# Kernel tuning notes

Measured on AMD Instinct MI355X. Metric: run time of the kernel, lower is better.

Reference implementation:

```python
import jax, jax.numpy as jnp
import numpy as np

K = 3            # kernel_size
H = 2048
W = 2048
N = 1_000_000    # number of query points
LATENT = 4
POS = 6
CTRL = 2
HID = 64
OUT = 4
IN_CH = (LATENT + POS + CTRL) * K * K  # 108


def _linear_params(key, fan_in, fan_out):
    bound = 1.0 / np.sqrt(fan_in)
    kw, kb = jax.random.split(key)
    Wm = jax.random.uniform(kw, (fan_in, fan_out), minval=-bound, maxval=bound, dtype=jnp.float32)
    bm = jax.random.uniform(kb, (fan_out,), minval=-bound, maxval=bound, dtype=jnp.float32)
    return Wm, bm


def setup_inputs() -> dict:
    key = jax.random.key(0)
    ks = jax.random.split(key, 7)
    W1, b1 = _linear_params(ks[0], IN_CH, HID)
    W2, b2 = _linear_params(ks[1], HID, 2 * HID)
    W3, b3 = _linear_params(ks[2], 2 * HID, HID)
    W4, b4 = _linear_params(ks[3], HID, OUT)
    latent = jax.random.normal(ks[4], (H, W, LATENT), dtype=jnp.float32)
    raw_pos = jax.random.randint(ks[5], (N, 2), 0, W).astype(jnp.int32)  # (x, y) coords
    control = jax.random.normal(ks[6], (N, CTRL), dtype=jnp.float32)
    return {"latent": latent, "raw_pos": raw_pos, "control": control,
            "W1": W1, "b1": b1, "W2": W2, "b2": b2,
            "W3": W3, "b3": b3, "W4": W4, "b4": b4}


def reference(latent, raw_pos, control, W1, b1, W2, b2, W3, b3, W4, b4):
    Hh, Ww, C = latent.shape
    n = raw_pos.shape[0]
    r = K // 2
    d = jnp.arange(-r, r + 1, dtype=raw_pos.dtype)
    ox, oy = jnp.meshgrid(d, d, indexing="xy")
    offsets = jnp.stack([ox.ravel(), oy.ravel()], axis=-1)          # [K*K, 2] (dx, dy)
    exp = raw_pos[:, None, :] + offsets[None, :, :]                 # [N, K*K, 2]
    ex = jnp.clip(exp[..., 0], 0, Ww - 1)
    ey = jnp.clip(exp[..., 1], 0, Hh - 1)
    lin = ey * Ww + ex                                              # linear gather indices
    latent_values = latent.reshape(-1, C)[lin]                      # [N, K*K, C] irregular gather

    xs = jnp.clip(raw_pos[:, 0:1], 0, Ww - 1).astype(latent.dtype) / Ww
    ys = jnp.clip(raw_pos[:, 1:2], 0, Hh - 1).astype(latent.dtype) / Hh
    tp = jnp.asarray(2.0 * np.pi, latent.dtype)
    # sinusoidal encoding with input included: [x, y, sin(2pi x), cos(2pi x), sin(2pi y), cos(2pi y)] -> pos_channels=6
    pos = jnp.concatenate([xs, ys, jnp.sin(tp * xs), jnp.cos(tp * xs), jnp.sin(tp * ys), jnp.cos(tp * ys)], axis=-1)
    pos_e = jnp.broadcast_to(pos[:, None, :], (n, K * K, POS))
    ctl_e = jnp.broadcast_to(control[:, None, :], (n, K * K, control.shape[-1]))

    patches = jnp.concatenate([latent_values, pos_e, ctl_e], axis=-1)  # [N, K*K, 12]
    x = patches.reshape(n, -1)                                          # [N, 108]

    h = jax.nn.gelu(x @ W1 + b1, approximate=False)
    h = jax.nn.gelu(h @ W2 + b2, approximate=False)
    h = jax.nn.gelu(h @ W3 + b3, approximate=False)
    return jax.nn.sigmoid(h @ W4 + b4)                                  # [N, 4]
```

## Files before the change

kernel.cpp:

```cpp
#include <hip/hip_runtime.h>
#include <hip/hip_fp16.h>

typedef __attribute__((ext_vector_type(8))) _Float16 half8;
typedef __attribute__((ext_vector_type(4))) float f32x4;
typedef __attribute__((ext_vector_type(4))) unsigned int uint4v;

#define HGT 2048
#define WID 2048
#define NPTS 1000000
#define NTILES 3907
#define WBYTES 44096
#define BIAS_OFF 43008

__device__ __host__ inline int c64map(int k){
  return 16*(k>>5) + 32*((k&7)>>2) + 4*((k>>3)&3) + (k&3);
}
__device__ __host__ inline int c128map(int k){
  return 16*(k>>5) + 64*((k&7)>>2) + 4*((k>>3)&3) + (k&3);
}

__global__ void prepack_kernel(const float* __restrict__ W1, const float* __restrict__ b1,
                               const float* __restrict__ W2, const float* __restrict__ b2,
                               const float* __restrict__ W3, const float* __restrict__ b3,
                               const float* __restrict__ W4, const float* __restrict__ b4,
                               unsigned short* __restrict__ packed){
  int tid = blockIdx.x*256 + threadIdx.x;
  if (tid < 42*64) {
    int f = tid >> 6, l = tid & 63;
    int fr = l & 15, kg = l >> 4;
    int layer, mt, kk;
    if (f < 8)       { layer=1; mt=f>>1;      kk=f&1; }
    else if (f < 24) { layer=2; mt=(f-8)>>1;  kk=(f-8)&1; }
    else if (f < 40) { layer=3; mt=(f-24)>>2; kk=(f-24)&3; }
    else             { layer=4; mt=0;         kk=f-40; }
    unsigned short v16[8];
    #pragma unroll
    for (int e=0;e<8;e++){
      int k = kk*32 + kg*8 + e;
      int fout = mt*16 + fr;
      float v = 0.0f;
      if (layer==1) {
        if (k < 36)      { v = W1[((k>>2)*12 + (k&3))*64 + fout]; }
        else if (k < 42) { float s=0.f; for (int p=0;p<9;p++) s += W1[(p*12+4+(k-36))*64 + fout]; v=s; }
        else if (k < 44) { float s=0.f; for (int p=0;p<9;p++) s += W1[(p*12+10+(k-42))*64 + fout]; v=s; }
      } else if (layer==2) { v = W2[c64map(k)*128 + fout]; }
      else if (layer==3)   { v = W3[c128map(k)*64 + fout]; }
      else                 { v = (fr < 4) ? W4[c64map(k)*4 + fr] : 0.0f; }
      v16[e] = __half_as_ushort(__float2half(v));
    }
    unsigned short* dst = packed + (size_t)f*512 + (size_t)l*8;
    #pragma unroll
    for (int e=0;e<8;e++) dst[e] = v16[e];
  }
  int bt = tid - 42*64;
  if (bt >= 0 && bt < 272) {
    float v;
    if (bt < 64)       v = b1[bt];
    else if (bt < 192) v = b2[bt-64];
    else if (bt < 256) v = b3[bt-192];
    else               v = (bt-256 < 4) ? b4[bt-256] : 0.0f;
    ((float*)((char*)packed + BIAS_OFF))[bt] = v;
  }
}

__device__ inline unsigned pkf(float a, float b){
  return __builtin_bit_cast(unsigned, __builtin_amdgcn_cvt_pkrtz(a, b));
}
__device__ inline float gelu1(float x){
  const float x2 = x*x;
  const float z  = x * __builtin_fmaf(0.10294913f, x2, 2.3021164f);
  const float t  = __builtin_amdgcn_exp2f(z);
  const float r  = __builtin_amdgcn_rcpf(t + 1.0f);
  return __builtin_fmaf(-x, r, x);
}
__device__ inline unsigned gelu2_v(float a, float b){
  return pkf(gelu1(a), gelu1(b));
}
__device__ inline float fast_sigmoid(float x){
  return __builtin_amdgcn_rcpf(1.0f + __builtin_amdgcn_exp2f(-1.442695041f*x));
}

template<int MT,int KT,int DKT,int FB,int BO>
__device__ inline void layer2(const half8* __restrict__ Wfrag, const float* __restrict__ bias,
                              const uint4v* ia, const uint4v* ib,
                              uint4v* oa, uint4v* ob, int lane, int g){
  #pragma unroll
  for (int mt=0; mt<MT; mt++){
    const f32x4 bv = *(const f32x4*)(bias + BO + mt*16 + g*4);
    f32x4 a = bv, b = bv;
    #pragma unroll
    for (int kk=0; kk<KT; kk++){
      const half8 w = Wfrag[(FB + mt*KT + kk)*64 + lane];
      a = __builtin_amdgcn_mfma_f32_16x16x32_f16(w, __builtin_bit_cast(half8, ia[kk]), a, 0,0,0);
      b = __builtin_amdgcn_mfma_f32_16x16x32_f16(w, __builtin_bit_cast(half8, ib[kk]), b, 0,0,0);
    }
    oa[mt%DKT][(mt/DKT)*2+0] = gelu2_v(a[0], a[1]);
    oa[mt%DKT][(mt/DKT)*2+1] = gelu2_v(a[2], a[3]);
    ob[mt%DKT][(mt/DKT)*2+0] = gelu2_v(b[0], b[1]);
    ob[mt%DKT][(mt/DKT)*2+1] = gelu2_v(b[2], b[3]);
  }
}

__global__ __launch_bounds__(512, 6)
void decoder_kernel(const float* __restrict__ latent, const int* __restrict__ raw_pos,
                    const float* __restrict__ control, const unsigned short* __restrict__ packed,
                    float* __restrict__ out){
  __shared__ __attribute__((aligned(16))) char smem[WBYTES];
  const int tid = threadIdx.x;
  {
    const f32x4* src = (const f32x4*)packed;
    f32x4* dst = (f32x4*)smem;
    for (int i = tid; i < WBYTES/16; i += 512) dst[i] = src[i];
  }
  __syncthreads();

  const half8* Wfrag = (const half8*)smem;
  const float* bias  = (const float*)(smem + BIAS_OFF);
  const int wave = tid >> 6, lane = tid & 63;
  const int nlo = lane & 15, g = lane >> 4;
  const int pA = g*2, pB = g*2+1;
  const int qA = (pA>=3) + (pA>=6), qB = (pB>=3) + (pB>=6);
  const int dyA = qA-1, dxA = pA-3*qA-1;
  const int dyB = qB-1, dxB = pB-3*qB-1;

  const int tile = blockIdx.x;
  const int R0 = tile*256 + wave*32;
  if (R0 >= NPTS) return;

  uint4v bx0[2], bx1[2];
  #pragma unroll
  for (int jj=0; jj<2; jj++){
    const int prow = R0 + jj*16 + nlo;
    const int2 xy = ((const int2*)raw_pos)[prow];
    const int exA = min(max(xy.x + dxA, 0), WID-1);
    const int eyA = min(max(xy.y + dyA, 0), HGT-1);
    const int exB = min(max(xy.x + dxB, 0), WID-1);
    const int eyB = min(max(xy.y + dyB, 0), HGT-1);
    const f32x4 lA = *(const f32x4*)(latent + ((size_t)eyA*WID + exA)*4);
    const f32x4 lB = *(const f32x4*)(latent + ((size_t)eyB*WID + exB)*4);
    uint4v f0;
    f0.x = pkf(lA[0], lA[1]); f0.y = pkf(lA[2], lA[3]);
    f0.z = pkf(lB[0], lB[1]); f0.w = pkf(lB[2], lB[3]);

    const float xs = (float)xy.x * (1.0f/WID), ys = (float)xy.y * (1.0f/HGT);
    const float sx = __builtin_amdgcn_sinf(xs), cx = __builtin_amdgcn_cosf(xs);
    const float sy = __builtin_amdgcn_sinf(ys), cy = __builtin_amdgcn_cosf(ys);
    uint4v f1; f1.x = 0u; f1.y = 0u; f1.z = 0u; f1.w = 0u;
    if (g == 0){
      const int ex8 = min(xy.x + 1, WID-1), ey8 = min(xy.y + 1, HGT-1);
      const f32x4 l8 = *(const f32x4*)(latent + ((size_t)ey8*WID + ex8)*4);
      f1.x = pkf(l8[0], l8[1]); f1.y = pkf(l8[2], l8[3]);
      f1.z = pkf(xs, ys); f1.w = pkf(sx, cx);
    } else if (g == 1){
      const float2 ct = ((const float2*)control)[prow];
      f1.x = pkf(sy, cy); f1.y = pkf(ct.x, ct.y);
    }
    if (jj == 0){ bx0[0] = f0; bx0[1] = f1; }
    else        { bx1[0] = f0; bx1[1] = f1; }
  }

  uint4v h1a[2], h1b[2], h2a[4], h2b[4], h3a[2], h3b[2];
  layer2<4,2,2, 0,  0>(Wfrag, bias, bx0, bx1, h1a, h1b, lane, g);
  layer2<8,2,4, 8, 64>(Wfrag, bias, h1a, h1b, h2a, h2b, lane, g);
  layer2<4,4,2,24,192>(Wfrag, bias, h2a, h2b, h3a, h3b, lane, g);

  const f32x4 bv4 = *(const f32x4*)(bias + 256 + g*4);
  f32x4 a = bv4, b = bv4;
  #pragma unroll
  for (int kk=0; kk<2; kk++){
    const half8 w = Wfrag[(40+kk)*64 + lane];
    a = __builtin_amdgcn_mfma_f32_16x16x32_f16(w, __builtin_bit_cast(half8, h3a[kk]), a, 0,0,0);
    b = __builtin_amdgcn_mfma_f32_16x16x32_f16(w, __builtin_bit_cast(half8, h3b[kk]), b, 0,0,0);
  }
  if (g == 0){
    f32x4 oa, ob;
    #pragma unroll
    for (int j=0;j<4;j++){ oa[j] = fast_sigmoid(a[j]); ob[j] = fast_sigmoid(b[j]); }
    *(f32x4*)(out + (size_t)(R0 + nlo)*4)      = oa;
    *(f32x4*)(out + (size_t)(R0 + 16 + nlo)*4) = ob;
  }
}

extern "C" void kernel_launch(void* const* d_in, const int* in_sizes, int n_in,
                              void* d_out, int out_size, void* d_ws, size_t ws_size,
                              hipStream_t stream) {
  const float* latent  = (const float*)d_in[0];
  const int*   raw_pos = (const int*)d_in[1];
  const float* control = (const float*)d_in[2];
  const float* W1 = (const float*)d_in[3];
  const float* b1 = (const float*)d_in[4];
  const float* W2 = (const float*)d_in[5];
  const float* b2 = (const float*)d_in[6];
  const float* W3 = (const float*)d_in[7];
  const float* b3 = (const float*)d_in[8];
  const float* W4 = (const float*)d_in[9];
  const float* b4 = (const float*)d_in[10];
  unsigned short* packed = (unsigned short*)d_ws;

  prepack_kernel<<<12, 256, 0, stream>>>(W1,b1,W2,b2,W3,b3,W4,b4,packed);
  decoder_kernel<<<NTILES, 512, 0, stream>>>(latent, raw_pos, control, packed, (float*)d_out);
}
```

Baseline: 108.3 us.

## Process 64 points per wave to amortize weight fragment loads

Each wave now handles four 16-point groups instead of two, so every weight fragment read from LDS feeds four MFMAs instead of two. The grid is halved and occupancy bounds drop from 6 to 4 waves per SIMD to fit the larger register footprint. Tail handling clamps input rows and guards output stores. This cuts LDS weight traffic and the per-block weight staging cost, but lowers occupancy, which may hurt latency hiding for the random latent gathers.

```diff
diff --git a/kernel.cpp b/kernel.cpp
--- a/kernel.cpp
+++ b/kernel.cpp
@@ -8,7 +8,7 @@
 #define HGT 2048
 #define WID 2048
 #define NPTS 1000000
-#define NTILES 3907
+#define NTILES 1954
 #define WBYTES 44096
 #define BIAS_OFF 43008
 
@@ -80,28 +80,32 @@
   return __builtin_amdgcn_rcpf(1.0f + __builtin_amdgcn_exp2f(-1.442695041f*x));
 }
 
-template<int MT,int KT,int DKT,int FB,int BO>
-__device__ inline void layer2(const half8* __restrict__ Wfrag, const float* __restrict__ bias,
-                              const uint4v* ia, const uint4v* ib,
-                              uint4v* oa, uint4v* ob, int lane, int g){
+template<int MT,int KT,int DKT,int FB,int BO,int J,int KIN>
+__device__ __forceinline__ void layerJ(const half8* __restrict__ Wfrag, const float* __restrict__ bias,
+                                       const uint4v (&in)[J][KIN], uint4v (&outp)[J][DKT],
+                                       int lane, int g){
   #pragma unroll
   for (int mt=0; mt<MT; mt++){
     const f32x4 bv = *(const f32x4*)(bias + BO + mt*16 + g*4);
-    f32x4 a = bv, b = bv;
+    f32x4 acc[J];
+    #pragma unroll
+    for (int j=0;j<J;j++) acc[j] = bv;
     #pragma unroll
     for (int kk=0; kk<KT; kk++){
       const half8 w = Wfrag[(FB + mt*KT + kk)*64 + lane];
-      a = __builtin_amdgcn_mfma_f32_16x16x32_f16(w, __builtin_bit_cast(half8, ia[kk]), a, 0,0,0);
-      b = __builtin_amdgcn_mfma_f32_16x16x32_f16(w, __builtin_bit_cast(half8, ib[kk]), b, 0,0,0);
-    }
-    oa[mt%DKT][(mt/DKT)*2+0] = gelu2_v(a[0], a[1]);
-    oa[mt%DKT][(mt/DKT)*2+1] = gelu2_v(a[2], a[3]);
-    ob[mt%DKT][(mt/DKT)*2+0] = gelu2_v(b[0], b[1]);
-    ob[mt%DKT][(mt/DKT)*2+1] = gelu2_v(b[2], b[3]);
-  }
-}
-
-__global__ __launch_bounds__(512, 6)
+      #pragma unroll
+      for (int j=0;j<J;j++)
+        acc[j] = __builtin_amdgcn_mfma_f32_16x16x32_f16(w, __builtin_bit_cast(half8, in[j][kk]), acc[j], 0,0,0);
+    }
+    #pragma unroll
+    for (int j=0;j<J;j++){
+      outp[j][mt%DKT][(mt/DKT)*2+0] = gelu2_v(acc[j][0], acc[j][1]);
+      outp[j][mt%DKT][(mt/DKT)*2+1] = gelu2_v(acc[j][2], acc[j][3]);
+    }
+  }
+}
+
+__global__ __launch_bounds__(512, 4)
 void decoder_kernel(const float* __restrict__ latent, const int* __restrict__ raw_pos,
                     const float* __restrict__ control, const unsigned short* __restrict__ packed,
                     float* __restrict__ out){
@@ -123,14 +127,12 @@
   const int dyA = qA-1, dxA = pA-3*qA-1;
   const int dyB = qB-1, dxB = pB-3*qB-1;
 
-  const int tile = blockIdx.x;
-  const int R0 = tile*256 + wave*32;
-  if (R0 >= NPTS) return;
-
-  uint4v bx0[2], bx1[2];
-  #pragma unroll
-  for (int jj=0; jj<2; jj++){
-    const int prow = R0 + jj*16 + nlo;
+  const int R0 = blockIdx.x*512 + wave*64;
+
+  uint4v bx[4][2];
+  #pragma unroll
+  for (int jj=0; jj<4; jj++){
+    const int prow = min(R0 + jj*16 + nlo, NPTS-1);
     const int2 xy = ((const int2*)raw_pos)[prow];
     const int exA = min(max(xy.x + dxA, 0), WID-1);
     const int eyA = min(max(xy.y + dyA, 0), HGT-1);
@@ -155,29 +157,36 @@
       const float2 ct = ((const float2*)control)[prow];
       f1.x = pkf(sy, cy); f1.y = pkf(ct.x, ct.y);
     }
-    if (jj == 0){ bx0[0] = f0; bx0[1] = f1; }
-    else        { bx1[0] = f0; bx1[1] = f1; }
-  }
-
-  uint4v h1a[2], h1b[2], h2a[4], h2b[4], h3a[2], h3b[2];
-  layer2<4,2,2, 0,  0>(Wfrag, bias, bx0, bx1, h1a, h1b, lane, g);
-  layer2<8,2,4, 8, 64>(Wfrag, bias, h1a, h1b, h2a, h2b, lane, g);
-  layer2<4,4,2,24,192>(Wfrag, bias, h2a, h2b, h3a, h3b, lane, g);
+    bx[jj][0] = f0; bx[jj][1] = f1;
+  }
+
+  uint4v h1[4][2], h2[4][4], h3[4][2];
+  layerJ<4,2,2, 0,  0,4,2>(Wfrag, bias, bx, h1, lane, g);
+  layerJ<8,2,4, 8, 64,4,2>(Wfrag, bias, h1, h2, lane, g);
+  layerJ<4,4,2,24,192,4,4>(Wfrag, bias, h2, h3, lane, g);
 
   const f32x4 bv4 = *(const f32x4*)(bias + 256 + g*4);
-  f32x4 a = bv4, b = bv4;
+  f32x4 acc[4];
+  #pragma unroll
+  for (int j=0;j<4;j++) acc[j] = bv4;
   #pragma unroll
   for (int kk=0; kk<2; kk++){
     const half8 w = Wfrag[(40+kk)*64 + lane];
-    a = __builtin_amdgcn_mfma_f32_16x16x32_f16(w, __builtin_bit_cast(half8, h3a[kk]), a, 0,0,0);
-    b = __builtin_amdgcn_mfma_f32_16x16x32_f16(w, __builtin_bit_cast(half8, h3b[kk]), b, 0,0,0);
+    #pragma unroll
+    for (int j=0;j<4;j++)
+      acc[j] = __builtin_amdgcn_mfma_f32_16x16x32_f16(w, __builtin_bit_cast(half8, h3[j][kk]), acc[j], 0,0,0);
   }
   if (g == 0){
-    f32x4 oa, ob;
-    #pragma unroll
-    for (int j=0;j<4;j++){ oa[j] = fast_sigmoid(a[j]); ob[j] = fast_sigmoid(b[j]); }
-    *(f32x4*)(out + (size_t)(R0 + nlo)*4)      = oa;
-    *(f32x4*)(out + (size_t)(R0 + 16 + nlo)*4) = ob;
+    #pragma unroll
+    for (int j=0;j<4;j++){
+      const int base = R0 + j*16;
+      if (base < NPTS){
+        f32x4 o;
+        #pragma unroll
+        for (int q=0;q<4;q++) o[q] = fast_sigmoid(acc[j][q]);
+        *(f32x4*)(out + (size_t)(base + nlo)*4) = o;
+      }
+    }
   }
 }
 
```

Result: slower. 117.1 us (+8.1%).
